# Optimization experiments

Hardware: AMD Instinct MI355X
Metric: run time of the kernel (lower is better)

## Reference

```python
import jax, jax.numpy as jnp
import numpy as np

WB = 8   # weight bit width (signed int8, power-of-two scale)
AB = 8   # activation bit width (uint8, power-of-two scale)
BB = 8   # bias bit width

# (name, c_in, c_out, kernel) for every QuantConv2d in order
_CFG = [("1", 3, 32, 3), ("2", 32, 16, 3), ("31", 16, 16, 1), ("32", 16, 32, 3),
        ("33", 32, 32, 1), ("34", 32, 64, 3), ("41", 64, 32, 1), ("42", 32, 64, 3),
        ("43", 64, 32, 1), ("44", 32, 64, 3), ("45", 64, 32, 1), ("46", 32, 64, 3)]
_POOL_AFTER = {"1", "2", "34"}  # MaxPool2d(2,2) follows these blocks


def _ste_round(x):
    # straight-through rounding (Brevitas-style fake quant)
    return x + jax.lax.stop_gradient(jnp.round(x) - x)


def _p2_scale(maxv, levels):
    # power-of-two (fixed point) per-tensor scale covering maxv with `levels` steps
    maxv = jnp.maximum(jax.lax.stop_gradient(maxv), 1e-8)
    return 2.0 ** jnp.ceil(jnp.log2(maxv / levels))


def quant_int(x, bw):
    # signed symmetric fixed-point fake quant (Int8WeightPerTensorFixedPoint style)
    n = 2.0 ** (bw - 1) - 1.0
    s = _p2_scale(jnp.max(jnp.abs(x)), n)
    return jnp.clip(_ste_round(x / s), -n - 1.0, n) * s


def quant_uint(x, bw):
    # unsigned fixed-point fake quant (Uint8ActPerTensorFixedPoint style)
    n = 2.0 ** bw - 1.0
    s = _p2_scale(jnp.max(x), n)
    return jnp.clip(_ste_round(x / s), 0.0, n) * s


def _conv(x, w, pad):
    return jax.lax.conv_general_dilated(
        x, w, window_strides=(1, 1), padding=[(pad, pad), (pad, pad)],
        dimension_numbers=("NCHW", "OIHW", "NCHW"))


def _maxpool2(x):
    return jax.lax.reduce_window(x, -jnp.inf, jax.lax.max,
                                 (1, 1, 2, 2), (1, 1, 2, 2), "VALID")


def _forward(x, p):
    # QuantIdentity on input (uint8 fixed point)
    x = quant_uint(x, AB)
    for n, ci, co, k in _CFG:
        pad = (k - 1) // 2
        y = _conv(x, quant_int(p["w" + n], WB), pad)               # quantized conv, no bias
        # BatchNorm2dToQuantScaleBias: per-channel affine with quantized scale/bias
        y = (y * quant_int(p["sg" + n], WB)[None, :, None, None]
             + quant_int(p["sb" + n], BB)[None, :, None, None])
        x = quant_uint(jax.nn.relu(y), AB)                          # QuantReLU
        if n in _POOL_AFTER:
            x = _maxpool2(x)
    # TruncAvgPool2d(28,28) over the remaining 28x28 map + RoundTo8bit requant
    x = quant_uint(jnp.mean(x, axis=(2, 3)), 8)                     # [B, 64]
    h = x @ quant_int(p["fw1"], WB).T + quant_int(p["fb1"], BB)     # linear51
    h = quant_uint(jax.nn.relu(h), AB)                              # relu5
    return h @ quant_int(p["fw2"], WB).T + quant_int(p["fb2"], BB)  # linear52


def setup_inputs() -> dict:
    key = jax.random.key(0)
    ks = iter(jax.random.split(key, 64))
    inp = {"x": jax.random.uniform(next(ks), (16, 3, 224, 224), jnp.float32)}
    for n, ci, co, k in _CFG:
        inp["w" + n] = jax.random.normal(next(ks), (co, ci, k, k), jnp.float32) * 0.1
        inp["sg" + n] = jax.random.uniform(next(ks), (co,), jnp.float32, 0.5, 1.5)
        inp["sb" + n] = jax.random.normal(next(ks), (co,), jnp.float32) * 0.1
    inp["fw1"] = jax.random.normal(next(ks), (16, 64), jnp.float32) * 0.1
    inp["fb1"] = jax.random.normal(next(ks), (16,), jnp.float32) * 0.1
    inp["fw2"] = jax.random.normal(next(ks), (10, 16), jnp.float32) * 0.1
    inp["fb2"] = jax.random.normal(next(ks), (10,), jnp.float32) * 0.1
    return inp


def reference(x, w1, sg1, sb1, w2, sg2, sb2, w31, sg31, sb31, w32, sg32, sb32,
              w33, sg33, sb33, w34, sg34, sb34, w41, sg41, sb41, w42, sg42, sb42,
              w43, sg43, sb43, w44, sg44, sb44, w45, sg45, sb45, w46, sg46, sb46,
              fw1, fb1, fw2, fb2):
    p = dict(locals())
    x = p.pop("x")
    return _forward(x, p)
```

## Files before the change

### kernel.cpp

```cpp
#include <hip/hip_runtime.h>
#include <math.h>

#define NL 12

typedef short v8s __attribute__((ext_vector_type(8)));
typedef float v4f __attribute__((ext_vector_type(4)));

struct PrepArgs {
  const float* in[40];
  void* out[40];
  int n[40];
  int mode[40];
  int tc[40];
  int ci[40], kk[40], kp[40], co[40];
};

__device__ inline float p2_scale_f(float maxv, float levels) {
  float r = __fdiv_rn(fmaxf(maxv, 1e-8f), levels);
  return (float)exp2(ceil(log2((double)r)));
}

__device__ inline float block_reduce_max256(float v) {
  __shared__ float sm[4];
  #pragma unroll
  for (int off = 32; off; off >>= 1) v = fmaxf(v, __shfl_down(v, off));
  if ((threadIdx.x & 63) == 0) sm[threadIdx.x >> 6] = v;
  __syncthreads();
  if (threadIdx.x == 0) v = fmaxf(fmaxf(sm[0], sm[1]), fmaxf(sm[2], sm[3]));
  return v;
}

__device__ inline void slot_max_update(float* slot, float v) {
  volatile unsigned int* su = (volatile unsigned int*)slot;
  unsigned int bits = __float_as_uint(v);
  if (bits > *su) atomicMax((unsigned int*)slot, bits);
}

__device__ inline short ibf16(float v) {
  return (short)(__float_as_uint(v) >> 16);
}

__global__ void prep_kernel(PrepArgs a, float* wslot,
                            const float* __restrict__ x, int nx, float* slot0) {
  if (blockIdx.x >= 40) {
    float m = 0.f;
    for (int i = (blockIdx.x - 40) * 256 + threadIdx.x; i < nx;
         i += (gridDim.x - 40) * 256)
      m = fmaxf(m, x[i]);
    float bm = block_reduce_max256(m);
    if (threadIdx.x == 0) slot_max_update(slot0, bm);
    return;
  }
  __shared__ float ssc;
  const int t = blockIdx.x;
  const float* in = a.in[t];
  const int n = a.n[t], mode = a.mode[t];
  float m = 0.f;
  for (int i = threadIdx.x; i < n; i += 256) m = fmaxf(m, fabsf(in[i]));
  float bm = block_reduce_max256(m);
  if (threadIdx.x == 0) {
    ssc = p2_scale_f(bm, 127.0f);
    if (mode == 2) wslot[t] = ssc;
  }
  __syncthreads();
  const float s = ssc;
  if (mode == 2) {
    ushort* o = (ushort*)a.out[t];
    const int CI = a.ci[t], KK = a.kk[t], KP = a.kp[t], CO = a.co[t];
    const int KT = CI * KK;
    for (int i = threadIdx.x; i < CO * KP; i += 256) {
      int co = i / KP, k = i % KP;
      ushort v = 0;
      if (k < KT) {
        int khkw = k / CI, ci = k % CI;
        float q = rintf(__fdiv_rn(in[(co * CI + ci) * KK + khkw], s));
        q = fminf(fmaxf(q, -128.f), 127.f);
        v = (ushort)(__float_as_uint(q) >> 16);
      }
      o[i] = v;
    }
  } else {
    float* o = (float*)a.out[t];
    const int tc = a.tc[t];
    const int nw = (mode == 1) ? n / tc : 1;
    for (int i = threadIdx.x; i < n; i += 256) {
      float q = rintf(__fdiv_rn(in[i], s));
      q = fminf(fmaxf(q, -128.f), 127.f);
      float v = __fmul_rn(q, s);
      if (mode == 1) o[(i % nw) * tc + i / nw] = v;
      else o[i] = v;
    }
  }
}


template <int CI, int H, int CO, bool K3, bool POOL>
__global__ __launch_bounds__(256)
void conv_mfma(const float* __restrict__ in, const short* __restrict__ wt,
               const float* __restrict__ sg, const float* __restrict__ sb,
               float* __restrict__ out, const float* __restrict__ slot_in,
               const float* __restrict__ wslotp, float* slot_out) {
  constexpr int W = H;
  constexpr int KT = (K3 ? 9 : 1) * CI;
  constexpr int SLABS = (KT + 31) / 32;
  constexpr int KP = SLABS * 32;
  constexpr int COT = CO / 16;
  constexpr int HO = POOL ? H / 2 : H;
  constexpr int WO = POOL ? W / 2 : W;

  const int lane = threadIdx.x & 63, widx = threadIdx.x >> 6;
  const int quad = lane >> 4, col = lane & 15;
  const float s_in = p2_scale_f(slot_in[0], 255.0f);
  const float inv = __fdiv_rn(1.0f, s_in);
  const float S = __fmul_rn(s_in, wslotp[0]);
  const int wv = blockIdx.x * 4 + widx;

  int n, h, w, ph = 0, pw = 0;
  if constexpr (POOL) {
    constexpr int PB = (HO / 2) * (WO / 2);
    n = wv / PB; int r = wv % PB;
    ph = r / (WO / 2); pw = r % (WO / 2);
    h = 4 * ph + (col >> 2); w = 4 * pw + (col & 3);
  } else {
    int p = wv * 16 + col;
    n = p / (H * W); int r = p % (H * W);
    h = r / W; w = r % W;
  }
  const float* ibase = in + (size_t)n * H * W * CI;

  v4f acc[COT];
  #pragma unroll
  for (int c = 0; c < COT; c++) acc[c] = (v4f){0.f, 0.f, 0.f, 0.f};

  #pragma unroll
  for (int slab = 0; slab < SLABS; slab++) {
    const int kbase = slab * 32 + quad * 8;
    v8s a;
    if constexpr (K3) {
      int khkw = kbase / CI; khkw = min(khkw, 8);
      const int cib = kbase % CI;
      const int kh = khkw / 3, kw = khkw - kh * 3;
      const int hh = h + kh - 1, ww = w + kw - 1;
      const bool valid = (hh >= 0) && (hh < H) && (ww >= 0) && (ww < W) && (kbase < KT);
      const int hc = min(max(hh, 0), H - 1), wc = min(max(ww, 0), W - 1);
      const float* ap = ibase + (size_t)(hc * W + wc) * CI + cib;
      float4 f0 = ((const float4*)ap)[0];
      float4 f1 = ((const float4*)ap)[1];
      float ff[8] = {f0.x, f0.y, f0.z, f0.w, f1.x, f1.y, f1.z, f1.w};
      #pragma unroll
      for (int j = 0; j < 8; j++) {
        float q = rintf(__fmul_rn(ff[j], inv));
        a[j] = valid ? ibf16(q) : (short)0;
      }
    } else {
      const int cib = kbase % CI;
      const float* ap = ibase + (size_t)(h * W + w) * CI + cib;
      float4 f0 = ((const float4*)ap)[0];
      float4 f1 = ((const float4*)ap)[1];
      float ff[8] = {f0.x, f0.y, f0.z, f0.w, f1.x, f1.y, f1.z, f1.w};
      #pragma unroll
      for (int j = 0; j < 8; j++) a[j] = ibf16(rintf(__fmul_rn(ff[j], inv)));
    }
    #pragma unroll
    for (int c = 0; c < COT; c++) {
      v8s b = *(const v8s*)(wt + (size_t)(c * 16 + col) * KP + kbase);
      acc[c] = __builtin_amdgcn_mfma_f32_16x16x32_bf16(a, b, acc[c], 0, 0, 0);
    }
  }

  float zmax = 0.f;
  #pragma unroll
  for (int c = 0; c < COT; c++) {
    const int cog = c * 16 + col;
    const float g = sg[cog], bb = sb[cog];
    float z[4];
    #pragma unroll
    for (int r2 = 0; r2 < 4; r2++) {
      float t = __fmul_rn(acc[c][r2], S);
      z[r2] = fmaxf(__fadd_rn(__fmul_rn(t, g), bb), 0.f);
    }
    if constexpr (POOL) {
      float h0 = fmaxf(z[0], z[1]), h1 = fmaxf(z[2], z[3]);
      float o0 = fmaxf(h0, __shfl_xor(h0, 16));
      float o1 = fmaxf(h1, __shfl_xor(h1, 16));
      zmax = fmaxf(zmax, fmaxf(o0, o1));
      if (!(quad & 1)) {
        int oh = 2 * ph + (quad >> 1), ow = 2 * pw;
        float* op = out + ((size_t)((n * HO + oh) * WO + ow)) * CO + cog;
        op[0] = o0; op[CO] = o1;
      }
    } else {
      const int pbase = wv * 16 + quad * 4;
      #pragma unroll
      for (int r2 = 0; r2 < 4; r2++) {
        out[(size_t)(pbase + r2) * CO + cog] = z[r2];
        zmax = fmaxf(zmax, z[r2]);
      }
    }
  }
  float bm = block_reduce_max256(zmax);
  if (threadIdx.x == 0) slot_max_update(slot_out, bm);
}

__global__ __launch_bounds__(256)
void conv1_mfma(const float* __restrict__ x, const short* __restrict__ wt,
                const float* __restrict__ sg, const float* __restrict__ sb,
                float* __restrict__ out, const float* __restrict__ slot_in,
                const float* __restrict__ wslotp, float* slot_out) {
  const int lane = threadIdx.x & 63, widx = threadIdx.x >> 6;
  const int quad = lane >> 4, col = lane & 15;
  const float s_in = p2_scale_f(slot_in[0], 255.0f);
  const float inv = __fdiv_rn(1.0f, s_in);
  const float S = __fmul_rn(s_in, wslotp[0]);
  const int wv = blockIdx.x * 4 + widx;
  const int n = wv / 3136, r = wv % 3136;
  const int ph = r / 56, pw = r % 56;
  const int h = 4 * ph + (col >> 2), w = 4 * pw + (col & 3);

  v8s a;
  #pragma unroll
  for (int j = 0; j < 8; j++) {
    int k = quad * 8 + j;
    int kc = min(k, 26);
    int khkw = kc / 3, ci = kc - khkw * 3;
    int kh = khkw / 3, kw = khkw - kh * 3;
    int hh = h + kh - 1, ww = w + kw - 1;
    bool valid = (k < 27) && (hh >= 0) && (hh < 224) && (ww >= 0) && (ww < 224);
    int hc = min(max(hh, 0), 223), wc = min(max(ww, 0), 223);
    float v = x[((n * 3 + ci) * 224 + hc) * 224 + wc];
    float q = rintf(__fmul_rn(v, inv));
    a[j] = valid ? ibf16(q) : (short)0;
  }
  v4f acc[2];
  acc[0] = (v4f){0.f, 0.f, 0.f, 0.f};
  acc[1] = acc[0];
  #pragma unroll
  for (int c = 0; c < 2; c++) {
    v8s b = *(const v8s*)(wt + (size_t)(c * 16 + col) * 32 + quad * 8);
    acc[c] = __builtin_amdgcn_mfma_f32_16x16x32_bf16(a, b, acc[c], 0, 0, 0);
  }
  float zmax = 0.f;
  #pragma unroll
  for (int c = 0; c < 2; c++) {
    const int cog = c * 16 + col;
    const float g = sg[cog], bb = sb[cog];
    float z[4];
    #pragma unroll
    for (int r2 = 0; r2 < 4; r2++) {
      float t = __fmul_rn(acc[c][r2], S);
      z[r2] = fmaxf(__fadd_rn(__fmul_rn(t, g), bb), 0.f);
    }
    float h0 = fmaxf(z[0], z[1]), h1 = fmaxf(z[2], z[3]);
    float o0 = fmaxf(h0, __shfl_xor(h0, 16));
    float o1 = fmaxf(h1, __shfl_xor(h1, 16));
    zmax = fmaxf(zmax, fmaxf(o0, o1));
    if (!(quad & 1)) {
      int oh = 2 * ph + (quad >> 1), ow = 2 * pw;
      float* op = out + ((size_t)((n * 112 + oh) * 112 + ow)) * 32 + cog;
      op[0] = o0; op[32] = o1;
    }
  }
  float bm = block_reduce_max256(zmax);
  if (threadIdx.x == 0) slot_max_update(slot_out, bm);
}

__global__ void avgpool_kernel(const float* __restrict__ in, float* __restrict__ out,
                               const float* __restrict__ slot_in, float* slot_out) {
  __shared__ float red[256];
  const float s = p2_scale_f(slot_in[0], 255.0f);
  const float inv = __fdiv_rn(1.0f, s);
  const int nn = blockIdx.x, co = threadIdx.x & 63, part = threadIdx.x >> 6;
  const float* p = in + (size_t)nn * 784 * 64;
  float sum = 0.f;
  for (int i = part * 196; i < part * 196 + 196; i++)
    sum += __fmul_rn(rintf(__fmul_rn(p[i * 64 + co], inv)), s);
  red[threadIdx.x] = sum;
  __syncthreads();
  if (threadIdx.x < 64) {
    float tot = (red[co] + red[64 + co]) + (red[128 + co] + red[192 + co]);
    float m = __fdiv_rn(tot, 784.0f);
    out[nn * 64 + co] = m;
    slot_max_update(slot_out, m);
  }
}

__global__ void tail_kernel(const float* __restrict__ pooled,
                            const float* __restrict__ fw1, const float* __restrict__ fb1,
                            const float* __restrict__ fw2, const float* __restrict__ fb2,
                            const float* __restrict__ slot_in, float* __restrict__ out) {
  __shared__ float xq[1024];
  __shared__ float hq[256];
  __shared__ float s2s;
  const int t = threadIdx.x;
  const float s = p2_scale_f(slot_in[0], 255.0f);
  const float inv = __fdiv_rn(1.0f, s);
  for (int i = t; i < 1024; i += 256)
    xq[i] = __fmul_rn(rintf(__fmul_rn(pooled[i], inv)), s);
  __syncthreads();
  const int n = t >> 4, j = t & 15;
  float acc = 0.f;
  #pragma unroll 8
  for (int k = 0; k < 64; k++) acc += xq[n * 64 + k] * fw1[k * 16 + j];
  float z = fmaxf(__fadd_rn(acc, fb1[j]), 0.f);
  float bm = block_reduce_max256(z);
  if (t == 0) s2s = p2_scale_f(bm, 255.0f);
  __syncthreads();
  const float s2 = s2s, inv2 = __fdiv_rn(1.0f, s2);
  hq[t] = __fmul_rn(rintf(__fmul_rn(z, inv2)), s2);
  __syncthreads();
  if (t < 160) {
    const int n2 = t / 10, j2 = t % 10;
    float a2 = 0.f;
    #pragma unroll
    for (int k = 0; k < 16; k++) a2 += hq[n2 * 16 + k] * fw2[k * 10 + j2];
    out[t] = __fadd_rn(a2, fb2[j2]);
  }
}

extern "C" void kernel_launch(void* const* d_in, const int* in_sizes, int n_in,
                              void* d_out, int out_size, void* d_ws, size_t ws_size,
                              hipStream_t stream) {
  static const int h_ci[NL] = {3, 32, 16, 16, 32, 32, 64, 32, 64, 32, 64, 32};
  static const int h_co[NL] = {32, 16, 16, 32, 32, 64, 32, 64, 32, 64, 32, 64};
  static const int h_kk[NL] = {9, 9, 1, 9, 1, 9, 1, 9, 1, 9, 1, 9};
  static const int h_kp[NL] = {32, 288, 32, 160, 32, 288, 64, 288, 64, 288, 64, 288};

  float* ws = (float*)d_ws;
  float* slots = ws;
  float* wslot = ws + 16;
  size_t off = 32;

  short* wq[NL];
  for (int l = 0; l < NL; l++) {
    wq[l] = (short*)(ws + off);
    off += (size_t)(h_co[l] * h_kp[l] + 1) / 2;
  }
  float* sgq[NL]; float* sbq[NL];
  for (int l = 0; l < NL; l++) { sgq[l] = ws + off; off += 64; }
  for (int l = 0; l < NL; l++) { sbq[l] = ws + off; off += 64; }
  float* fw1q = ws + off; off += 1024;
  float* fb1q = ws + off; off += 16;
  float* fw2q = ws + off; off += 160;
  float* fb2q = ws + off; off += 16;
  float* A = ws + off; off += 6422528;
  float* B = ws + off; off += 1605632;
  float* P = ws + off; off += 1024;

  PrepArgs pa;
  for (int l = 0; l < NL; l++) {
    pa.in[l] = (const float*)d_in[1 + 3 * l]; pa.out[l] = (void*)wq[l];
    pa.n[l] = h_co[l] * h_ci[l] * h_kk[l];
    pa.mode[l] = 2; pa.tc[l] = 0;
    pa.ci[l] = h_ci[l]; pa.kk[l] = h_kk[l]; pa.kp[l] = h_kp[l]; pa.co[l] = h_co[l];
    pa.in[12 + l] = (const float*)d_in[2 + 3 * l]; pa.out[12 + l] = (void*)sgq[l];
    pa.n[12 + l] = h_co[l]; pa.mode[12 + l] = 0; pa.tc[12 + l] = 0;
    pa.ci[12 + l] = pa.kk[12 + l] = pa.kp[12 + l] = pa.co[12 + l] = 0;
    pa.in[24 + l] = (const float*)d_in[3 + 3 * l]; pa.out[24 + l] = (void*)sbq[l];
    pa.n[24 + l] = h_co[l]; pa.mode[24 + l] = 0; pa.tc[24 + l] = 0;
    pa.ci[24 + l] = pa.kk[24 + l] = pa.kp[24 + l] = pa.co[24 + l] = 0;
  }
  pa.in[36] = (const float*)d_in[37]; pa.out[36] = (void*)fw1q;
  pa.n[36] = 1024; pa.mode[36] = 1; pa.tc[36] = 16;
  pa.ci[36] = pa.kk[36] = pa.kp[36] = pa.co[36] = 0;
  pa.in[37] = (const float*)d_in[38]; pa.out[37] = (void*)fb1q;
  pa.n[37] = 16; pa.mode[37] = 0; pa.tc[37] = 0;
  pa.ci[37] = pa.kk[37] = pa.kp[37] = pa.co[37] = 0;
  pa.in[38] = (const float*)d_in[39]; pa.out[38] = (void*)fw2q;
  pa.n[38] = 160; pa.mode[38] = 1; pa.tc[38] = 10;
  pa.ci[38] = pa.kk[38] = pa.kp[38] = pa.co[38] = 0;
  pa.in[39] = (const float*)d_in[40]; pa.out[39] = (void*)fb2q;
  pa.n[39] = 10; pa.mode[39] = 0; pa.tc[39] = 0;
  pa.ci[39] = pa.kk[39] = pa.kp[39] = pa.co[39] = 0;

  const float* x = (const float*)d_in[0];
  const int nx = 16 * 3 * 224 * 224;

  hipMemsetAsync(slots, 0, 16 * sizeof(float), stream);
  prep_kernel<<<40 + 2048, 256, 0, stream>>>(pa, wslot, x, nx, slots + 0);

  conv1_mfma<<<12544, 256, 0, stream>>>(x, wq[0], sgq[0], sbq[0], A,
                                        slots + 0, wslot + 0, slots + 1);
  conv_mfma<32, 112, 16, true, true><<<3136, 256, 0, stream>>>(
      A, wq[1], sgq[1], sbq[1], B, slots + 1, wslot + 1, slots + 2);
  conv_mfma<16, 56, 16, false, false><<<784, 256, 0, stream>>>(
      B, wq[2], sgq[2], sbq[2], A, slots + 2, wslot + 2, slots + 3);
  conv_mfma<16, 56, 32, true, false><<<784, 256, 0, stream>>>(
      A, wq[3], sgq[3], sbq[3], B, slots + 3, wslot + 3, slots + 4);
  conv_mfma<32, 56, 32, false, false><<<784, 256, 0, stream>>>(
      B, wq[4], sgq[4], sbq[4], A, slots + 4, wslot + 4, slots + 5);
  conv_mfma<32, 56, 64, true, true><<<784, 256, 0, stream>>>(
      A, wq[5], sgq[5], sbq[5], B, slots + 5, wslot + 5, slots + 6);
  conv_mfma<64, 28, 32, false, false><<<196, 256, 0, stream>>>(
      B, wq[6], sgq[6], sbq[6], A, slots + 6, wslot + 6, slots + 7);
  conv_mfma<32, 28, 64, true, false><<<196, 256, 0, stream>>>(
      A, wq[7], sgq[7], sbq[7], B, slots + 7, wslot + 7, slots + 8);
  conv_mfma<64, 28, 32, false, false><<<196, 256, 0, stream>>>(
      B, wq[8], sgq[8], sbq[8], A, slots + 8, wslot + 8, slots + 9);
  conv_mfma<32, 28, 64, true, false><<<196, 256, 0, stream>>>(
      A, wq[9], sgq[9], sbq[9], B, slots + 9, wslot + 9, slots + 10);
  conv_mfma<64, 28, 32, false, false><<<196, 256, 0, stream>>>(
      B, wq[10], sgq[10], sbq[10], A, slots + 10, wslot + 10, slots + 11);
  conv_mfma<32, 28, 64, true, false><<<196, 256, 0, stream>>>(
      A, wq[11], sgq[11], sbq[11], B, slots + 11, wslot + 11, slots + 12);

  avgpool_kernel<<<16, 256, 0, stream>>>(B, P, slots + 12, slots + 13);
  tail_kernel<<<1, 256, 0, stream>>>(P, fw1q, fb1q, fw2q, fb2q, slots + 13,
                                     (float*)d_out);
}
```

Baseline: 402.4 us.

## Pre-pack quantized activations to bf16 before each conv to shrink im2col reads

Adds a pack kernel before every conv layer that quantizes fp32 activations to bf16 integer codes once, so the conv kernels read half-width data and skip the per-tap rounding. This removes redundant requantization across the 9 taps of 3x3 convs. The 3x3 path now precomputes tap offsets and validity. The input max reduction is vectorized with float4 loads on fewer blocks. In exchange it adds 12 extra launches and an extra full write plus read of each activation tensor.

```diff
diff --git a/kernel.cpp b/kernel.cpp
--- a/kernel.cpp
+++ b/kernel.cpp
@@ -36,17 +36,18 @@
   if (bits > *su) atomicMax((unsigned int*)slot, bits);
 }
 
-__device__ inline short ibf16(float v) {
-  return (short)(__float_as_uint(v) >> 16);
+__device__ inline ushort ibf16(float v) {
+  return (ushort)(__float_as_uint(v) >> 16);
 }
 
 __global__ void prep_kernel(PrepArgs a, float* wslot,
-                            const float* __restrict__ x, int nx, float* slot0) {
+                            const float4* __restrict__ x4, int nx4, float* slot0) {
   if (blockIdx.x >= 40) {
     float m = 0.f;
-    for (int i = (blockIdx.x - 40) * 256 + threadIdx.x; i < nx;
-         i += (gridDim.x - 40) * 256)
-      m = fmaxf(m, x[i]);
+    for (int i = (blockIdx.x - 40) * 256 + threadIdx.x; i < nx4; i += 256 * 256) {
+      float4 v = x4[i];
+      m = fmaxf(fmaxf(fmaxf(m, v.x), fmaxf(v.y, v.z)), v.w);
+    }
     float bm = block_reduce_max256(m);
     if (threadIdx.x == 0) slot_max_update(slot0, bm);
     return;
@@ -75,7 +76,7 @@
         int khkw = k / CI, ci = k % CI;
         float q = rintf(__fdiv_rn(in[(co * CI + ci) * KK + khkw], s));
         q = fminf(fmaxf(q, -128.f), 127.f);
-        v = (ushort)(__float_as_uint(q) >> 16);
+        v = ibf16(q);
       }
       o[i] = v;
     }
@@ -93,10 +94,28 @@
   }
 }
 
+__global__ void pack_kernel(const float4* __restrict__ in, ushort* __restrict__ out,
+                            int n4, const float* __restrict__ slot) {
+  __shared__ float sinv;
+  if (threadIdx.x == 0) sinv = __fdiv_rn(1.0f, p2_scale_f(slot[0], 255.0f));
+  __syncthreads();
+  const float inv = sinv;
+  const int i = blockIdx.x * 256 + threadIdx.x;
+  if (i < n4) {
+    float4 v = in[i];
+    ushort4 o;
+    o.x = ibf16(rintf(__fmul_rn(v.x, inv)));
+    o.y = ibf16(rintf(__fmul_rn(v.y, inv)));
+    o.z = ibf16(rintf(__fmul_rn(v.z, inv)));
+    o.w = ibf16(rintf(__fmul_rn(v.w, inv)));
+    ((ushort4*)out)[i] = o;
+  }
+}
+
 
 template <int CI, int H, int CO, bool K3, bool POOL>
 __global__ __launch_bounds__(256)
-void conv_mfma(const float* __restrict__ in, const short* __restrict__ wt,
+void conv_mfma(const ushort* __restrict__ in, const ushort* __restrict__ wt,
                const float* __restrict__ sg, const float* __restrict__ sb,
                float* __restrict__ out, const float* __restrict__ slot_in,
                const float* __restrict__ wslotp, float* slot_out) {
@@ -107,11 +126,12 @@
   constexpr int COT = CO / 16;
   constexpr int HO = POOL ? H / 2 : H;
   constexpr int WO = POOL ? W / 2 : W;
+  static_assert(!K3 || CI == 16 || CI == 32, "K3 path assumes CI 16/32");
 
   const int lane = threadIdx.x & 63, widx = threadIdx.x >> 6;
   const int quad = lane >> 4, col = lane & 15;
+  __builtin_assume(quad >= 0 && quad < 4);
   const float s_in = p2_scale_f(slot_in[0], 255.0f);
-  const float inv = __fdiv_rn(1.0f, s_in);
   const float S = __fmul_rn(s_in, wslotp[0]);
   const int wv = blockIdx.x * 4 + widx;
 
@@ -126,44 +146,48 @@
     n = p / (H * W); int r = p % (H * W);
     h = r / W; w = r % W;
   }
-  const float* ibase = in + (size_t)n * H * W * CI;
+  const ushort* ibase = in + (size_t)n * H * W * CI;
+
+  int toff[10]; bool tval[10];
+  if constexpr (K3) {
+    #pragma unroll
+    for (int t = 0; t < 9; t++) {
+      int kh = t / 3, kw = t % 3;
+      int hh = h + kh - 1, ww = w + kw - 1;
+      tval[t] = (hh >= 0) && (hh < H) && (ww >= 0) && (ww < W);
+      toff[t] = (min(max(hh, 0), H - 1) * W + min(max(ww, 0), W - 1)) * CI;
+    }
+    toff[9] = toff[8]; tval[9] = false;
+  }
 
   v4f acc[COT];
   #pragma unroll
   for (int c = 0; c < COT; c++) acc[c] = (v4f){0.f, 0.f, 0.f, 0.f};
+  const v8s zv = {0, 0, 0, 0, 0, 0, 0, 0};
 
   #pragma unroll
   for (int slab = 0; slab < SLABS; slab++) {
-    const int kbase = slab * 32 + quad * 8;
     v8s a;
     if constexpr (K3) {
-      int khkw = kbase / CI; khkw = min(khkw, 8);
-      const int cib = kbase % CI;
-      const int kh = khkw / 3, kw = khkw - kh * 3;
-      const int hh = h + kh - 1, ww = w + kw - 1;
-      const bool valid = (hh >= 0) && (hh < H) && (ww >= 0) && (ww < W) && (kbase < KT);
-      const int hc = min(max(hh, 0), H - 1), wc = min(max(ww, 0), W - 1);
-      const float* ap = ibase + (size_t)(hc * W + wc) * CI + cib;
-      float4 f0 = ((const float4*)ap)[0];
-      float4 f1 = ((const float4*)ap)[1];
-      float ff[8] = {f0.x, f0.y, f0.z, f0.w, f1.x, f1.y, f1.z, f1.w};
-      #pragma unroll
-      for (int j = 0; j < 8; j++) {
-        float q = rintf(__fmul_rn(ff[j], inv));
-        a[j] = valid ? ibf16(q) : (short)0;
+      int tof; bool tv;
+      int cib;
+      if constexpr (CI == 32) {
+        tof = toff[slab]; tv = tval[slab]; cib = quad * 8;
+      } else {
+        const bool hi = (quad & 2) != 0;
+        tof = hi ? toff[2 * slab + 1] : toff[2 * slab];
+        tv  = hi ? tval[2 * slab + 1] : tval[2 * slab];
+        cib = (quad & 1) * 8;
       }
+      v8s av = *(const v8s*)(ibase + tof + cib);
+      a = tv ? av : zv;
     } else {
-      const int cib = kbase % CI;
-      const float* ap = ibase + (size_t)(h * W + w) * CI + cib;
-      float4 f0 = ((const float4*)ap)[0];
-      float4 f1 = ((const float4*)ap)[1];
-      float ff[8] = {f0.x, f0.y, f0.z, f0.w, f1.x, f1.y, f1.z, f1.w};
-      #pragma unroll
-      for (int j = 0; j < 8; j++) a[j] = ibf16(rintf(__fmul_rn(ff[j], inv)));
+      const int cib = (slab * 32 + quad * 8) % CI;
+      a = *(const v8s*)(ibase + (size_t)(h * W + w) * CI + cib);
     }
     #pragma unroll
     for (int c = 0; c < COT; c++) {
-      v8s b = *(const v8s*)(wt + (size_t)(c * 16 + col) * KP + kbase);
+      v8s b = *(const v8s*)(wt + (size_t)(c * 16 + col) * KP + slab * 32 + quad * 8);
       acc[c] = __builtin_amdgcn_mfma_f32_16x16x32_bf16(a, b, acc[c], 0, 0, 0);
     }
   }
@@ -203,14 +227,13 @@
 }
 
 __global__ __launch_bounds__(256)
-void conv1_mfma(const float* __restrict__ x, const short* __restrict__ wt,
+void conv1_mfma(const ushort* __restrict__ xc, const ushort* __restrict__ wt,
                 const float* __restrict__ sg, const float* __restrict__ sb,
                 float* __restrict__ out, const float* __restrict__ slot_in,
                 const float* __restrict__ wslotp, float* slot_out) {
   const int lane = threadIdx.x & 63, widx = threadIdx.x >> 6;
   const int quad = lane >> 4, col = lane & 15;
   const float s_in = p2_scale_f(slot_in[0], 255.0f);
-  const float inv = __fdiv_rn(1.0f, s_in);
   const float S = __fmul_rn(s_in, wslotp[0]);
   const int wv = blockIdx.x * 4 + widx;
   const int n = wv / 3136, r = wv % 3136;
@@ -227,9 +250,8 @@
     int hh = h + kh - 1, ww = w + kw - 1;
     bool valid = (k < 27) && (hh >= 0) && (hh < 224) && (ww >= 0) && (ww < 224);
     int hc = min(max(hh, 0), 223), wc = min(max(ww, 0), 223);
-    float v = x[((n * 3 + ci) * 224 + hc) * 224 + wc];
-    float q = rintf(__fmul_rn(v, inv));
-    a[j] = valid ? ibf16(q) : (short)0;
+    ushort v = xc[((n * 3 + ci) * 224 + hc) * 224 + wc];
+    a[j] = valid ? (short)v : (short)0;
   }
   v4f acc[2];
   acc[0] = (v4f){0.f, 0.f, 0.f, 0.f};
@@ -330,10 +352,10 @@
   float* wslot = ws + 16;
   size_t off = 32;
 
-  short* wq[NL];
+  ushort* wq[NL];
   for (int l = 0; l < NL; l++) {
-    wq[l] = (short*)(ws + off);
-    off += (size_t)(h_co[l] * h_kp[l] + 1) / 2;
+    wq[l] = (ushort*)(ws + off);
+    off += (size_t)(h_co[l] * h_kp[l]) / 2;
   }
   float* sgq[NL]; float* sbq[NL];
   for (int l = 0; l < NL; l++) { sgq[l] = ws + off; off += 64; }
@@ -342,8 +364,9 @@
   float* fb1q = ws + off; off += 16;
   float* fw2q = ws + off; off += 160;
   float* fb2q = ws + off; off += 16;
-  float* A = ws + off; off += 6422528;
-  float* B = ws + off; off += 1605632;
+  float* rawA = ws + off; off += 6422528;
+  float* rawB = ws + off; off += 1605632;
+  ushort* C  = (ushort*)(ws + off); off += 3211264;
   float* P = ws + off; off += 1024;
 
   PrepArgs pa;
@@ -373,37 +396,60 @@
   pa.ci[39] = pa.kk[39] = pa.kp[39] = pa.co[39] = 0;
 
   const float* x = (const float*)d_in[0];
-  const int nx = 16 * 3 * 224 * 224;
+  const int nx4 = 16 * 3 * 224 * 224 / 4;
 
   hipMemsetAsync(slots, 0, 16 * sizeof(float), stream);
-  prep_kernel<<<40 + 2048, 256, 0, stream>>>(pa, wslot, x, nx, slots + 0);
-
-  conv1_mfma<<<12544, 256, 0, stream>>>(x, wq[0], sgq[0], sbq[0], A,
+  prep_kernel<<<40 + 256, 256, 0, stream>>>(pa, wslot, (const float4*)x, nx4, slots + 0);
+
+  pack_kernel<<<2352, 256, 0, stream>>>((const float4*)x, C, nx4, slots + 0);
+  conv1_mfma<<<12544, 256, 0, stream>>>(C, wq[0], sgq[0], sbq[0], rawA,
                                         slots + 0, wslot + 0, slots + 1);
+
+  pack_kernel<<<6272, 256, 0, stream>>>((const float4*)rawA, C, 1605632, slots + 1);
   conv_mfma<32, 112, 16, true, true><<<3136, 256, 0, stream>>>(
-      A, wq[1], sgq[1], sbq[1], B, slots + 1, wslot + 1, slots + 2);
+      C, wq[1], sgq[1], sbq[1], rawB, slots + 1, wslot + 1, slots + 2);
+
+  pack_kernel<<<784, 256, 0, stream>>>((const float4*)rawB, C, 200704, slots + 2);
   conv_mfma<16, 56, 16, false, false><<<784, 256, 0, stream>>>(
-      B, wq[2], sgq[2], sbq[2], A, slots + 2, wslot + 2, slots + 3);
+      C, wq[2], sgq[2], sbq[2], rawA, slots + 2, wslot + 2, slots + 3);
+
+  pack_kernel<<<784, 256, 0, stream>>>((const float4*)rawA, C, 200704, slots + 3);
   conv_mfma<16, 56, 32, true, false><<<784, 256, 0, stream>>>(
-      A, wq[3], sgq[3], sbq[3], B, slots + 3, wslot + 3, slots + 4);
+      C, wq[3], sgq[3], sbq[3], rawB, slots + 3, wslot + 3, slots + 4);
+
+  pack_kernel<<<1568, 256, 0, stream>>>((const float4*)rawB, C, 401408, slots + 4);
   conv_mfma<32, 56, 32, false, false><<<784, 256, 0, stream>>>(
-      B, wq[4], sgq[4], sbq[4], A, slots + 4, wslot + 4, slots + 5);
+      C, wq[4], sgq[4], sbq[4], rawA, slots + 4, wslot + 4, slots + 5);
+
+  pack_kernel<<<1568, 256, 0, stream>>>((const float4*)rawA, C, 401408, slots + 5);
   conv_mfma<32, 56, 64, true, true><<<784, 256, 0, stream>>>(
-      A, wq[5], sgq[5], sbq[5], B, slots + 5, wslot + 5, slots + 6);
+      C, wq[5], sgq[5], sbq[5], rawB, slots + 5, wslot + 5, slots + 6);
+
+  pack_kernel<<<784, 256, 0, stream>>>((const float4*)rawB, C, 200704, slots + 6);
   conv_mfma<64, 28, 32, false, false><<<196, 256, 0, stream>>>(
-      B, wq[6], sgq[6], sbq[6], A, slots + 6, wslot + 6, slots + 7);
+      C, wq[6], sgq[6], sbq[6], rawA, slots + 6, wslot + 6, slots + 7);
+
+  pack_kernel<<<392, 256, 0, stream>>>((const float4*)rawA, C, 100352, slots + 7);
   conv_mfma<32, 28, 64, true, false><<<196, 256, 0, stream>>>(
-      A, wq[7], sgq[7], sbq[7], B, slots + 7, wslot + 7, slots + 8);
+      C, wq[7], sgq[7], sbq[7], rawB, slots + 7, wslot + 7, slots + 8);
+
+  pack_kernel<<<784, 256, 0, stream>>>((const float4*)rawB, C, 200704, slots + 8);
   conv_mfma<64, 28, 32, false, false><<<196, 256, 0, stream>>>(
-      B, wq[8], sgq[8], sbq[8], A, slots + 8, wslot + 8, slots + 9);
+      C, wq[8], sgq[8], sbq[8], rawA, slots + 8, wslot + 8, slots + 9);
+
+  pack_kernel<<<392, 256, 0, stream>>>((const float4*)rawA, C, 100352, slots + 9);
   conv_mfma<32, 28, 64, true, false><<<196, 256, 0, stream>>>(
-      A, wq[9], sgq[9], sbq[9], B, slots + 9, wslot + 9, slots + 10);
+      C, wq[9], sgq[9], sbq[9], rawB, slots + 9, wslot + 9, slots + 10);
+
+  pack_kernel<<<784, 256, 0, stream>>>((const float4*)rawB, C, 200704, slots + 10);
   conv_mfma<64, 28, 32, false, false><<<196, 256, 0, stream>>>(
-      B, wq[10], sgq[10], sbq[10], A, slots + 10, wslot + 10, slots + 11);
+      C, wq[10], sgq[10], sbq[10], rawA, slots + 10, wslot + 10, slots + 11);
+
+  pack_kernel<<<392, 256, 0, stream>>>((const float4*)rawA, C, 100352, slots + 11);
   conv_mfma<32, 28, 64, true, false><<<196, 256, 0, stream>>>(
-      A, wq[11], sgq[11], sbq[11], B, slots + 11, wslot + 11, slots + 12);
-
-  avgpool_kernel<<<16, 256, 0, stream>>>(B, P, slots + 12, slots + 13);
+      C, wq[11], sgq[11], sbq[11], rawB, slots + 11, wslot + 11, slots + 12);
+
+  avgpool_kernel<<<16, 256, 0, stream>>>(rawB, P, slots + 12, slots + 13);
   tail_kernel<<<1, 256, 0, stream>>>(P, fw1q, fb1q, fw2q, fb2q, slots + 13,
                                      (float*)d_out);
 }
```

New measurement: 422.9 us. 1.05x slower.
